# Kernel tuning notes

Hardware: AMD Instinct MI355X
Metric: run time of the kernel (lower is better)

## Reference

```python
import jax, jax.numpy as jnp
import numpy as np

TEMPERATURE = 0.07
EPS = 1e-08
HARD_NEG_WEIGHT = 2.0
DOMAIN_SEP_WEIGHT = 1.5


def setup_inputs() -> dict:
    key = jax.random.key(0)
    k1, k2, k3 = jax.random.split(key, 3)
    B, L, D = 32, 256, 256
    feats = jax.random.normal(k1, (B, L, D), dtype=jnp.float32)
    dataset_ids = jax.random.randint(k2, (B, L), 0, 4, dtype=jnp.int64 if jax.config.read('jax_enable_x64') else jnp.int32)
    image_ids = jax.random.randint(k3, (B, L), 0, 128, dtype=jnp.int64 if jax.config.read('jax_enable_x64') else jnp.int32)
    return {"feats": feats, "dataset_ids": dataset_ids, "image_ids": image_ids}


def reference(feats, dataset_ids, image_ids):
    B, L, D = feats.shape
    N = B * L
    x = feats.reshape(N, D)
    # F.normalize: x / clamp_min(||x||, eps)
    x = x / jnp.maximum(jnp.linalg.norm(x, axis=-1, keepdims=True), EPS)
    sim = jnp.matmul(x, x.T) / TEMPERATURE  # [N, N]

    did = dataset_ids.reshape(-1)
    iid = image_ids.reshape(-1)
    same_img = (did[:, None] == did[None, :]) & (iid[:, None] == iid[None, :])
    eye = jnp.eye(N, dtype=bool)
    pos_mask = same_img & ~eye
    diff_dataset = did[:, None] != did[None, :]

    sim_exp = jnp.exp(sim)

    # global 0.8-quantile over cross-dataset similarities (linear interpolation, as torch.quantile)
    q = jnp.nanquantile(jnp.where(diff_dataset, sim, jnp.nan), 0.8)
    thr = jnp.where(diff_dataset.any(), q, 0.0)
    hard_neg_mask = diff_dataset & (sim > thr)

    neg_weights = jnp.where(diff_dataset, DOMAIN_SEP_WEIGHT, 1.0) * jnp.where(hard_neg_mask, HARD_NEG_WEIGHT, 1.0)

    pos_sum = jnp.sum(sim_exp * pos_mask.astype(sim.dtype), axis=1)
    # note: ~pos_mask includes the diagonal, matching the torch code
    neg_sum = jnp.sum(sim_exp * neg_weights * (~pos_mask).astype(sim.dtype), axis=1)

    loss = -jnp.log((pos_sum + EPS) / (pos_sum + neg_sum + EPS))

    valid = pos_mask.any(axis=1)
    n_valid = valid.sum()
    masked_mean = jnp.sum(loss * valid.astype(loss.dtype)) / jnp.maximum(n_valid, 1).astype(loss.dtype)
    return jnp.where(n_valid > 0, masked_mean, loss.mean())
```

## Files before the change

kernel.cpp:

```cpp
#include <hip/hip_runtime.h>
#include <hip/hip_bf16.h>
#include <math.h>

#define N_TOK 8192
#define DIM   256
#define INV_T 14.285714285714286f
#define RANGE 14.2857142857f
#define EPS   1e-8f
#define NBINS 8192
#define LOG2E 1.44269504f

typedef __attribute__((ext_vector_type(4))) float f32x4;
typedef __attribute__((ext_vector_type(8))) short short8;

#define OFF_P     0
#define P_BYTES   (N_TOK * DIM * 2)
#define OFF_PP    (OFF_P + P_BYTES)
#define OFF_PN    (OFF_PP + 64 * N_TOK * 4)
#define OFF_HIST  (OFF_PN + 64 * N_TOK * 4)
#define OFF_THR   (OFF_HIST + NBINS * 4)
#define WS_USED   (OFF_THR + 256)

#define GLOBAL_AS __attribute__((address_space(1)))
#define LDS_AS    __attribute__((address_space(3)))

__device__ __forceinline__ void tri_decode(int b, int& it, int& jt) {
    int i_low = (int)((sqrtf(8.f * (float)b + 1.f) - 1.f) * 0.5f);
    while ((i_low + 1) * (i_low + 2) / 2 <= b) ++i_low;
    while (i_low * (i_low + 1) / 2 > b) --i_low;
    const int j_low = b - i_low * (i_low + 1) / 2;
    it = 63 - i_low; jt = 63 - j_low;
}

__global__ __launch_bounds__(256) void k_prep(const float* __restrict__ feats,
                                              __hip_bfloat16* __restrict__ P) {
    const int row = blockIdx.x * 4 + (threadIdx.x >> 6);
    const int l = threadIdx.x & 63;
    const float4 v = *reinterpret_cast<const float4*>(&feats[(size_t)row * DIM + l * 4]);
    float s = v.x * v.x + v.y * v.y + v.z * v.z + v.w * v.w;
#pragma unroll
    for (int m = 1; m <= 32; m <<= 1) s += __shfl_xor(s, m);
    const float r = 1.0f / fmaxf(sqrtf(s), EPS);
    ushort4 o;
    __hip_bfloat16 h;
    h = __float2bfloat16(v.x * r); o.x = *reinterpret_cast<unsigned short*>(&h);
    h = __float2bfloat16(v.y * r); o.y = *reinterpret_cast<unsigned short*>(&h);
    h = __float2bfloat16(v.z * r); o.z = *reinterpret_cast<unsigned short*>(&h);
    h = __float2bfloat16(v.w * r); o.w = *reinterpret_cast<unsigned short*>(&h);
    *reinterpret_cast<ushort4*>(&P[(size_t)row * DIM + l * 4]) = o;
}

__global__ __launch_bounds__(512, 4) void k_hist(
    const __hip_bfloat16* __restrict__ P, const int* __restrict__ did,
    unsigned int* __restrict__ hist) {
    int it, jt;
    tri_decode(blockIdx.x, it, jt);
    if (((it * 67 + jt * 31) & 31) != 0) return;
    const int iBase = it * 128, jBase = jt * 128;
    const bool diag = (it == jt);

    __shared__ __hip_bfloat16 At[128 * 64];
    __shared__ __hip_bfloat16 Bt[128 * 64];
    __shared__ int dA[128], dB[128];
    __shared__ unsigned int h[NBINS];

    const int tid = threadIdx.x;
    const int w = tid >> 6, l = tid & 63;
    const int wr = w >> 1, wc = w & 1;
    const int g = l >> 4, p = l & 15;

    if (tid < 128) dA[tid] = did[iBase + tid];
    else if (tid < 256) dB[tid - 128] = did[jBase + tid - 128];
    for (int i = tid; i < NBINS; i += 512) h[i] = 0;

    f32x4 acc[2][4];
#pragma unroll
    for (int a = 0; a < 2; a++)
#pragma unroll
        for (int c = 0; c < 4; c++) acc[a][c] = (f32x4){0.f, 0.f, 0.f, 0.f};

    const int rloc = l >> 3;
    const int swz = (((l & 7) ^ (rloc & 7)) << 4);
    const char* Pb = (const char*)P;

    for (int t = 0; t < 4; ++t) {
#pragma unroll
        for (int i_ = 0; i_ < 2; ++i_) {
            const int rowbase = w * 16 + i_ * 8;
            const char* srcA = Pb + (size_t)(iBase + rowbase + rloc) * 512 + t * 128 + swz;
            __builtin_amdgcn_global_load_lds(
                (const GLOBAL_AS unsigned int*)srcA,
                (LDS_AS unsigned int*)(&At[rowbase * 64]), 16, 0, 0);
            const char* srcB = Pb + (size_t)(jBase + rowbase + rloc) * 512 + t * 128 + swz;
            __builtin_amdgcn_global_load_lds(
                (const GLOBAL_AS unsigned int*)srcB,
                (LDS_AS unsigned int*)(&Bt[rowbase * 64]), 16, 0, 0);
        }
        __syncthreads();
#pragma unroll
        for (int ks = 0; ks < 2; ++ks) {
            short8 af[2], bf[4];
            const int cb = ks * 64 + (g << 4);
#pragma unroll
            for (int fm = 0; fm < 2; ++fm) {
                const int row = wr * 32 + fm * 16 + p;
                af[fm] = *reinterpret_cast<const short8*>(
                    (const char*)At + row * 128 + (cb ^ ((row & 7) << 4)));
            }
#pragma unroll
            for (int fn = 0; fn < 4; ++fn) {
                const int row = wc * 64 + fn * 16 + p;
                bf[fn] = *reinterpret_cast<const short8*>(
                    (const char*)Bt + row * 128 + (cb ^ ((row & 7) << 4)));
            }
#pragma unroll
            for (int fm = 0; fm < 2; ++fm)
#pragma unroll
                for (int fn = 0; fn < 4; ++fn)
                    acc[fm][fn] = __builtin_amdgcn_mfma_f32_16x16x32_bf16(
                        af[fm], bf[fn], acc[fm][fn], 0, 0, 0);
        }
        __syncthreads();
    }

    int dRow[2][4];
#pragma unroll
    for (int fm = 0; fm < 2; ++fm)
#pragma unroll
        for (int q = 0; q < 4; ++q) dRow[fm][q] = dA[wr * 32 + fm * 16 + g * 4 + q];

    const unsigned int wgt = diag ? 1u : 2u;
    const float binScale = (float)NBINS / (2.0f * RANGE);
    const float K1 = INV_T * binScale, K0 = RANGE * binScale;
#pragma unroll
    for (int fn = 0; fn < 4; ++fn) {
        const int dcol = dB[wc * 64 + fn * 16 + p];
#pragma unroll
        for (int fm = 0; fm < 2; ++fm)
#pragma unroll
            for (int q = 0; q < 4; ++q) {
                if (dRow[fm][q] != dcol) {
                    int bn = (int)fmaf(acc[fm][fn][q], K1, K0);
                    bn = min(max(bn, 0), NBINS - 1);
                    atomicAdd(&h[bn], wgt);
                }
            }
    }
    __syncthreads();
    for (int i = tid; i < NBINS; i += 512) {
        unsigned int c = h[i];
        if (c) atomicAdd(&hist[i], c);
    }
}

__global__ __launch_bounds__(512, 8) void k_main(
    const __hip_bfloat16* __restrict__ P,
    const int* __restrict__ did, const int* __restrict__ iid,
    const float* __restrict__ thrp,
    float* __restrict__ partP, float* __restrict__ partN) {
    int it, jt;
    tri_decode(blockIdx.x, it, jt);
    const int iBase = it * 128, jBase = jt * 128;
    const bool diag = (it == jt);

    __shared__ __hip_bfloat16 At[2][128 * 32];
    __shared__ __hip_bfloat16 Bt[2][128 * 32];
    __shared__ int dA[128], kA[128], dB[128], kB[128];
    __shared__ float rbT[2][128], rbP[2][128];
    __shared__ float cbT[4][128], cbP[4][128];

    const int tid = threadIdx.x;
    const int w = tid >> 6, l = tid & 63;
    const int wr = w >> 1, wc = w & 1;
    const int g = l >> 4, p = l & 15;

    if (tid < 128) {
        int d = did[iBase + tid], i2 = iid[iBase + tid];
        dA[tid] = d; kA[tid] = (d << 16) | i2;
    } else if (tid < 256) {
        int r = tid - 128;
        int d = did[jBase + r], i2 = iid[jBase + r];
        dB[r] = d; kB[r] = (d << 16) | i2;
    }

    f32x4 acc[2][4];
#pragma unroll
    for (int a = 0; a < 2; a++)
#pragma unroll
        for (int c = 0; c < 4; c++) acc[a][c] = (f32x4){0.f, 0.f, 0.f, 0.f};

    const int rloc = l >> 2;
    const int swzB = (((l & 3) ^ (rloc & 3)) << 4);
    const char* Pb = (const char*)P;

#define STAGE(buf, t)                                                             \
    {                                                                             \
        const int row_ = w * 16 + rloc;                                           \
        const char* srcA_ = Pb + (size_t)(iBase + row_) * 512 + (t) * 64 + swzB;  \
        __builtin_amdgcn_global_load_lds(                                         \
            (const GLOBAL_AS unsigned int*)srcA_,                                 \
            (LDS_AS unsigned int*)(&At[buf][(w * 16) * 32]), 16, 0, 0);           \
        const char* srcB_ = Pb + (size_t)(jBase + row_) * 512 + (t) * 64 + swzB;  \
        __builtin_amdgcn_global_load_lds(                                         \
            (const GLOBAL_AS unsigned int*)srcB_,                                 \
            (LDS_AS unsigned int*)(&Bt[buf][(w * 16) * 32]), 16, 0, 0);           \
    }

    STAGE(0, 0);
    __syncthreads();

    for (int t = 0; t < 8; ++t) {
        const int cur = t & 1;
        if (t < 7) STAGE(cur ^ 1, t + 1);
        short8 af[2], bf[4];
        const int cbg = g << 4;
#pragma unroll
        for (int fm = 0; fm < 2; ++fm) {
            const int row = wr * 32 + fm * 16 + p;
            af[fm] = *reinterpret_cast<const short8*>(
                (const char*)At[cur] + row * 64 + (cbg ^ ((row & 3) << 4)));
        }
#pragma unroll
        for (int fn = 0; fn < 4; ++fn) {
            const int row = wc * 64 + fn * 16 + p;
            bf[fn] = *reinterpret_cast<const short8*>(
                (const char*)Bt[cur] + row * 64 + (cbg ^ ((row & 3) << 4)));
        }
#pragma unroll
        for (int fm = 0; fm < 2; ++fm)
#pragma unroll
            for (int fn = 0; fn < 4; ++fn)
                acc[fm][fn] = __builtin_amdgcn_mfma_f32_16x16x32_bf16(
                    af[fm], bf[fn], acc[fm][fn], 0, 0, 0);
        __syncthreads();
    }
#undef STAGE

    int dRow[2][4], kRow[2][4], selfRow[2][4];
#pragma unroll
    for (int fm = 0; fm < 2; ++fm)
#pragma unroll
        for (int q = 0; q < 4; ++q) {
            const int rIdx = wr * 32 + fm * 16 + g * 4 + q;
            dRow[fm][q] = dA[rIdx];
            kRow[fm][q] = kA[rIdx];
            selfRow[fm][q] = diag ? rIdx : -1;
        }

    const float CE = INV_T * LOG2E;
    const float thr2 = thrp[0] * LOG2E;
    float tR[2][4], pR[2][4], tC[4], pC[4];
#pragma unroll
    for (int a = 0; a < 4; a++) { tC[a] = 0.f; pC[a] = 0.f; }
#pragma unroll
    for (int a = 0; a < 2; a++)
#pragma unroll
        for (int c = 0; c < 4; c++) { tR[a][c] = 0.f; pR[a][c] = 0.f; }

#pragma unroll
    for (int fn = 0; fn < 4; ++fn) {
        const int cIdx = wc * 64 + fn * 16 + p;
        const int dcol = dB[cIdx], kcol = kB[cIdx];
#pragma unroll
        for (int fm = 0; fm < 2; ++fm)
#pragma unroll
            for (int q = 0; q < 4; ++q) {
                const float tt = acc[fm][fn][q] * CE;
                const float e = __builtin_amdgcn_exp2f(tt);
                const float w1 = (tt > thr2) ? 3.0f : 1.5f;
                const float wg = (dRow[fm][q] != dcol) ? w1 : 1.0f;
                tR[fm][q] = fmaf(e, wg, tR[fm][q]);
                tC[fn] = fmaf(e, wg, tC[fn]);
                const bool pos = (kRow[fm][q] == kcol) && (selfRow[fm][q] != cIdx);
                const float ep = pos ? e : 0.f;
                pR[fm][q] += ep;
                pC[fn] += ep;
            }
    }
#pragma unroll
    for (int m = 1; m <= 8; m <<= 1)
#pragma unroll
        for (int a = 0; a < 2; a++)
#pragma unroll
            for (int c = 0; c < 4; c++) {
                tR[a][c] += __shfl_xor(tR[a][c], m);
                pR[a][c] += __shfl_xor(pR[a][c], m);
            }
#pragma unroll
    for (int m = 16; m <= 32; m <<= 1)
#pragma unroll
        for (int a = 0; a < 4; a++) {
            tC[a] += __shfl_xor(tC[a], m);
            pC[a] += __shfl_xor(pC[a], m);
        }
    float tv = 0.f, pv = 0.f;
#pragma unroll
    for (int fm = 0; fm < 2; ++fm)
#pragma unroll
        for (int q = 0; q < 4; ++q)
            if (p == fm * 4 + q) { tv = tR[fm][q]; pv = pR[fm][q]; }

    if (p < 8) {
        const int rowLocal = (p >> 2) * 16 + g * 4 + (p & 3);
        rbT[wc][wr * 32 + rowLocal] = tv;
        rbP[wc][wr * 32 + rowLocal] = pv;
    }
    if (l < 16) {
#pragma unroll
        for (int fn = 0; fn < 4; ++fn) {
            cbT[wr][wc * 64 + fn * 16 + l] = tC[fn];
            cbP[wr][wc * 64 + fn * 16 + l] = pC[fn];
        }
    }
    __syncthreads();
    if (tid < 128) {
        const float T = rbT[0][tid] + rbT[1][tid];
        const float Pp = rbP[0][tid] + rbP[1][tid];
        const size_t off = (size_t)jt * N_TOK + iBase + tid;
        partP[off] = Pp;
        partN[off] = T - Pp;
    } else if (tid < 256 && !diag) {
        const int c = tid - 128;
        const float T = cbT[0][c] + cbT[1][c] + cbT[2][c] + cbT[3][c];
        const float Pp = cbP[0][c] + cbP[1][c] + cbP[2][c] + cbP[3][c];
        const size_t off = (size_t)it * N_TOK + jBase + c;
        partP[off] = Pp;
        partN[off] = T - Pp;
    }
}

__global__ __launch_bounds__(1024) void k_thr(const unsigned int* __restrict__ hist,
                                              float* __restrict__ thrp) {
    __shared__ unsigned long long scan[1024];
    const int t = threadIdx.x;
    const int CHUNK = NBINS / 1024;
    const int base = t * CHUNK;
    unsigned long long own = 0;
    for (int i = 0; i < CHUNK; i++) own += hist[base + i];
    scan[t] = own;
    __syncthreads();
    for (int o = 1; o < 1024; o <<= 1) {
        unsigned long long v = (t >= o) ? scan[t - o] : 0ULL;
        __syncthreads();
        scan[t] += v;
        __syncthreads();
    }
    unsigned long long total = scan[1023];
    if (total == 0) {
        if (t == 0) thrp[0] = 0.f;
        return;
    }
    unsigned long long k1 = (4ULL * (total - 1)) / 5ULL;
    unsigned long long rem = (4ULL * (total - 1)) % 5ULL;
    float frac = (float)rem * 0.2f;
    unsigned long long k2 = (k1 + 1 < total) ? k1 + 1 : k1;
    __shared__ float vk[2];
    unsigned long long cumBefore = scan[t] - own;
    const float binw = 2.0f * RANGE / (float)NBINS;
    for (int which = 0; which < 2; which++) {
        unsigned long long k = which ? k2 : k1;
        if (cumBefore <= k && k < scan[t]) {
            unsigned long long c = cumBefore;
            int bin = base;
            for (int i = 0; i < CHUNK; i++) {
                c += hist[base + i];
                if (c > k) { bin = base + i; break; }
            }
            vk[which] = -RANGE + ((float)bin + 0.5f) * binw;
        }
    }
    __syncthreads();
    if (t == 0) thrp[0] = vk[0] + frac * (vk[1] - vk[0]);
}

__global__ __launch_bounds__(256) void k_reduce(const float* __restrict__ pp,
                                                const float* __restrict__ pn,
                                                float* __restrict__ acc) {
    const int t = threadIdx.x;
    const int r = blockIdx.x * 128 + (t & 127);
    const int jh = t >> 7;
    float sp = 0.f, sn = 0.f;
    const float* bp = pp + (size_t)jh * 32 * N_TOK + r;
    const float* bn = pn + (size_t)jh * 32 * N_TOK + r;
#pragma unroll 8
    for (int j = 0; j < 32; ++j) {
        sp += bp[(size_t)j * N_TOK];
        sn += bn[(size_t)j * N_TOK];
    }
    __shared__ float shp[128], shn[128];
    if (jh) { shp[t & 127] = sp; shn[t & 127] = sn; }
    __syncthreads();
    float sumV = 0.f, sumA = 0.f, cnt = 0.f;
    if (!jh) {
        const float p = sp + shp[t];
        const float n = sn + shn[t];
        const float loss = -logf((p + EPS) / (p + n + EPS));
        sumA = loss;
        if (p > 0.f) { sumV = loss; cnt = 1.f; }
    }
#pragma unroll
    for (int m = 1; m <= 32; m <<= 1) {
        sumV += __shfl_xor(sumV, m);
        sumA += __shfl_xor(sumA, m);
        cnt += __shfl_xor(cnt, m);
    }
    __shared__ float wv[4], wa[4], wn[4];
    if ((t & 63) == 0) { wv[t >> 6] = sumV; wa[t >> 6] = sumA; wn[t >> 6] = cnt; }
    __syncthreads();
    if (t == 0) {
        atomicAdd(&acc[0], wv[0] + wv[1] + wv[2] + wv[3]);
        atomicAdd(&acc[1], wa[0] + wa[1] + wa[2] + wa[3]);
        atomicAdd(&acc[2], wn[0] + wn[1] + wn[2] + wn[3]);
    }
}

__global__ __launch_bounds__(64) void k_last(const float* __restrict__ acc,
                                             float* __restrict__ out) {
    if (threadIdx.x == 0) {
        const float nv = acc[2];
        out[0] = (nv > 0.f) ? (acc[0] / fmaxf(nv, 1.f)) : (acc[1] / (float)N_TOK);
    }
}

extern "C" void kernel_launch(void* const* d_in, const int* in_sizes, int n_in,
                              void* d_out, int out_size, void* d_ws, size_t ws_size,
                              hipStream_t stream) {
    (void)in_sizes; (void)n_in; (void)out_size; (void)ws_size;
    const float* feats = (const float*)d_in[0];
    const int* did = (const int*)d_in[1];
    const int* iid = (const int*)d_in[2];
    char* ws = (char*)d_ws;
    __hip_bfloat16* P = (__hip_bfloat16*)(ws + OFF_P);
    float* partP = (float*)(ws + OFF_PP);
    float* partN = (float*)(ws + OFF_PN);
    unsigned int* hist = (unsigned int*)(ws + OFF_HIST);
    float* thrp = (float*)(ws + OFF_THR);
    float* accum = (float*)(ws + OFF_THR + 16);

    hipMemsetAsync(ws + OFF_HIST, 0, NBINS * 4 + 256, stream);
    k_prep<<<N_TOK / 4, 256, 0, stream>>>(feats, P);
    const int NTILES = 64 * 65 / 2;
    k_hist<<<NTILES, 512, 0, stream>>>(P, did, hist);
    k_thr<<<1, 1024, 0, stream>>>(hist, thrp);
    k_main<<<NTILES, 512, 0, stream>>>(P, did, iid, thrp, partP, partN);
    k_reduce<<<64, 256, 0, stream>>>(partP, partN, accum);
    k_last<<<1, 64, 0, stream>>>(accum, (float*)d_out);
}
```

Measured before the change: 79.26 us.

## Switch normalized features to FP8 and use single-stage FP8 MFMA GEMM

Quantizes the normalized features to FP8 instead of bf16 and runs the similarity GEMMs with FP8 MFMA instructions. The whole 128x256 tile for each operand is staged into padded LDS in one pass, replacing the double-buffered k-loop. The histogram kernel now launches only the sampled tiles (65 blocks) instead of launching every tile and exiting early. The diagonal exp is replaced with an exact constant to hide FP8 self-similarity error. FP8 precision can change the similarity values and the quantile threshold, which risks accuracy, and the larger LDS footprint lowers occupancy.

New measurement: 72.92 us. 8.0% less time.

```diff
diff --git a/kernel.cpp b/kernel.cpp
--- a/kernel.cpp
+++ b/kernel.cpp
@@ -1,5 +1,4 @@
 #include <hip/hip_runtime.h>
-#include <hip/hip_bf16.h>
 #include <math.h>
 
 #define N_TOK 8192
@@ -11,18 +10,20 @@
 #define LOG2E 1.44269504f
 
 typedef __attribute__((ext_vector_type(4))) float f32x4;
-typedef __attribute__((ext_vector_type(8))) short short8;
 
 #define OFF_P     0
-#define P_BYTES   (N_TOK * DIM * 2)
+#define P_BYTES   (N_TOK * DIM)
 #define OFF_PP    (OFF_P + P_BYTES)
 #define OFF_PN    (OFF_PP + 64 * N_TOK * 4)
 #define OFF_HIST  (OFF_PN + 64 * N_TOK * 4)
 #define OFF_THR   (OFF_HIST + NBINS * 4)
-#define WS_USED   (OFF_THR + 256)
 
 #define GLOBAL_AS __attribute__((address_space(1)))
 #define LDS_AS    __attribute__((address_space(3)))
+
+#define ROWB 272
+#define SLOTS_PER_MAT (128 * 17)
+#define STAGE_CALLS (2 * SLOTS_PER_MAT / 64)
 
 __device__ __forceinline__ void tri_decode(int b, int& it, int& jt) {
     int i_low = (int)((sqrtf(8.f * (float)b + 1.f) - 1.f) * 0.5f);
@@ -33,7 +34,7 @@
 }
 
 __global__ __launch_bounds__(256) void k_prep(const float* __restrict__ feats,
-                                              __hip_bfloat16* __restrict__ P) {
+                                              unsigned int* __restrict__ Pq) {
     const int row = blockIdx.x * 4 + (threadIdx.x >> 6);
     const int l = threadIdx.x & 63;
     const float4 v = *reinterpret_cast<const float4*>(&feats[(size_t)row * DIM + l * 4]);
@@ -41,88 +42,83 @@
 #pragma unroll
     for (int m = 1; m <= 32; m <<= 1) s += __shfl_xor(s, m);
     const float r = 1.0f / fmaxf(sqrtf(s), EPS);
-    ushort4 o;
-    __hip_bfloat16 h;
-    h = __float2bfloat16(v.x * r); o.x = *reinterpret_cast<unsigned short*>(&h);
-    h = __float2bfloat16(v.y * r); o.y = *reinterpret_cast<unsigned short*>(&h);
-    h = __float2bfloat16(v.z * r); o.z = *reinterpret_cast<unsigned short*>(&h);
-    h = __float2bfloat16(v.w * r); o.w = *reinterpret_cast<unsigned short*>(&h);
-    *reinterpret_cast<ushort4*>(&P[(size_t)row * DIM + l * 4]) = o;
-}
-
-__global__ __launch_bounds__(512, 4) void k_hist(
-    const __hip_bfloat16* __restrict__ P, const int* __restrict__ did,
+    int pk = __builtin_amdgcn_cvt_pk_fp8_f32(v.x * r, v.y * r, 0, false);
+    pk = __builtin_amdgcn_cvt_pk_fp8_f32(v.z * r, v.w * r, pk, true);
+    Pq[row * 64 + l] = (unsigned int)pk;
+}
+
+__device__ __forceinline__ void stage_and_gemm(
+    const char* __restrict__ Pq, int iBase, int jBase,
+    char* At, char* Bt, int tid, f32x4 (&acc)[2][4]) {
+    const int w = tid >> 6, l = tid & 63;
+    for (int k = w; k < STAGE_CALLS; k += 8) {
+        const int s0 = k * 64;
+        const int isB = (s0 >= SLOTS_PER_MAT);
+        const int r0 = s0 - (isB ? SLOTS_PER_MAT : 0);
+        const int sl = r0 + l;
+        const int row = sl / 17;
+        const int col = sl - row * 17;
+        const int gb = isB ? jBase : iBase;
+        const char* src = Pq + (size_t)(gb + row) * DIM + (col & 15) * 16;
+        char* dst = (isB ? Bt : At) + (size_t)r0 * 16;
+        __builtin_amdgcn_global_load_lds((const GLOBAL_AS unsigned int*)src,
+                                         (LDS_AS unsigned int*)dst, 16, 0, 0);
+    }
+    __syncthreads();
+
+    const int wr = w >> 1, wc = w & 1;
+    const int g = l >> 4, p = l & 15;
+    const char* a0 = At + (wr * 32 + p) * ROWB + g * 8;
+    const char* b0 = Bt + (wc * 64 + p) * ROWB + g * 8;
+#pragma unroll
+    for (int c = 0; c < 8; ++c) {
+        const int off = c * 32;
+        const long af0 = *(const long*)(a0 + off);
+        const long af1 = *(const long*)(a0 + 16 * ROWB + off);
+        const long bf0 = *(const long*)(b0 + off);
+        const long bf1 = *(const long*)(b0 + 16 * ROWB + off);
+        const long bf2 = *(const long*)(b0 + 32 * ROWB + off);
+        const long bf3 = *(const long*)(b0 + 48 * ROWB + off);
+        acc[0][0] = __builtin_amdgcn_mfma_f32_16x16x32_fp8_fp8(af0, bf0, acc[0][0], 0, 0, 0);
+        acc[0][1] = __builtin_amdgcn_mfma_f32_16x16x32_fp8_fp8(af0, bf1, acc[0][1], 0, 0, 0);
+        acc[0][2] = __builtin_amdgcn_mfma_f32_16x16x32_fp8_fp8(af0, bf2, acc[0][2], 0, 0, 0);
+        acc[0][3] = __builtin_amdgcn_mfma_f32_16x16x32_fp8_fp8(af0, bf3, acc[0][3], 0, 0, 0);
+        acc[1][0] = __builtin_amdgcn_mfma_f32_16x16x32_fp8_fp8(af1, bf0, acc[1][0], 0, 0, 0);
+        acc[1][1] = __builtin_amdgcn_mfma_f32_16x16x32_fp8_fp8(af1, bf1, acc[1][1], 0, 0, 0);
+        acc[1][2] = __builtin_amdgcn_mfma_f32_16x16x32_fp8_fp8(af1, bf2, acc[1][2], 0, 0, 0);
+        acc[1][3] = __builtin_amdgcn_mfma_f32_16x16x32_fp8_fp8(af1, bf3, acc[1][3], 0, 0, 0);
+    }
+}
+
+__global__ __launch_bounds__(512, 2) void k_hist(
+    const char* __restrict__ Pq, const int* __restrict__ did,
     unsigned int* __restrict__ hist) {
     int it, jt;
-    tri_decode(blockIdx.x, it, jt);
-    if (((it * 67 + jt * 31) & 31) != 0) return;
+    tri_decode(blockIdx.x * 32, it, jt);
     const int iBase = it * 128, jBase = jt * 128;
     const bool diag = (it == jt);
 
-    __shared__ __hip_bfloat16 At[128 * 64];
-    __shared__ __hip_bfloat16 Bt[128 * 64];
+    __shared__ char At[SLOTS_PER_MAT * 16];
+    __shared__ char Bt[SLOTS_PER_MAT * 16];
     __shared__ int dA[128], dB[128];
     __shared__ unsigned int h[NBINS];
 
     const int tid = threadIdx.x;
+    if (tid < 128) dA[tid] = did[iBase + tid];
+    else if (tid < 256) dB[tid - 128] = did[jBase + tid - 128];
+    for (int i = tid; i < NBINS; i += 512) h[i] = 0;
+
+    f32x4 acc[2][4];
+#pragma unroll
+    for (int a = 0; a < 2; a++)
+#pragma unroll
+        for (int c = 0; c < 4; c++) acc[a][c] = (f32x4){0.f, 0.f, 0.f, 0.f};
+
+    stage_and_gemm(Pq, iBase, jBase, At, Bt, tid, acc);
+
     const int w = tid >> 6, l = tid & 63;
     const int wr = w >> 1, wc = w & 1;
     const int g = l >> 4, p = l & 15;
-
-    if (tid < 128) dA[tid] = did[iBase + tid];
-    else if (tid < 256) dB[tid - 128] = did[jBase + tid - 128];
-    for (int i = tid; i < NBINS; i += 512) h[i] = 0;
-
-    f32x4 acc[2][4];
-#pragma unroll
-    for (int a = 0; a < 2; a++)
-#pragma unroll
-        for (int c = 0; c < 4; c++) acc[a][c] = (f32x4){0.f, 0.f, 0.f, 0.f};
-
-    const int rloc = l >> 3;
-    const int swz = (((l & 7) ^ (rloc & 7)) << 4);
-    const char* Pb = (const char*)P;
-
-    for (int t = 0; t < 4; ++t) {
-#pragma unroll
-        for (int i_ = 0; i_ < 2; ++i_) {
-            const int rowbase = w * 16 + i_ * 8;
-            const char* srcA = Pb + (size_t)(iBase + rowbase + rloc) * 512 + t * 128 + swz;
-            __builtin_amdgcn_global_load_lds(
-                (const GLOBAL_AS unsigned int*)srcA,
-                (LDS_AS unsigned int*)(&At[rowbase * 64]), 16, 0, 0);
-            const char* srcB = Pb + (size_t)(jBase + rowbase + rloc) * 512 + t * 128 + swz;
-            __builtin_amdgcn_global_load_lds(
-                (const GLOBAL_AS unsigned int*)srcB,
-                (LDS_AS unsigned int*)(&Bt[rowbase * 64]), 16, 0, 0);
-        }
-        __syncthreads();
-#pragma unroll
-        for (int ks = 0; ks < 2; ++ks) {
-            short8 af[2], bf[4];
-            const int cb = ks * 64 + (g << 4);
-#pragma unroll
-            for (int fm = 0; fm < 2; ++fm) {
-                const int row = wr * 32 + fm * 16 + p;
-                af[fm] = *reinterpret_cast<const short8*>(
-                    (const char*)At + row * 128 + (cb ^ ((row & 7) << 4)));
-            }
-#pragma unroll
-            for (int fn = 0; fn < 4; ++fn) {
-                const int row = wc * 64 + fn * 16 + p;
-                bf[fn] = *reinterpret_cast<const short8*>(
-                    (const char*)Bt + row * 128 + (cb ^ ((row & 7) << 4)));
-            }
-#pragma unroll
-            for (int fm = 0; fm < 2; ++fm)
-#pragma unroll
-                for (int fn = 0; fn < 4; ++fn)
-                    acc[fm][fn] = __builtin_amdgcn_mfma_f32_16x16x32_bf16(
-                        af[fm], bf[fn], acc[fm][fn], 0, 0, 0);
-        }
-        __syncthreads();
-    }
-
     int dRow[2][4];
 #pragma unroll
     for (int fm = 0; fm < 2; ++fm)
@@ -153,8 +149,8 @@
     }
 }
 
-__global__ __launch_bounds__(512, 8) void k_main(
-    const __hip_bfloat16* __restrict__ P,
+__global__ __launch_bounds__(512, 4) void k_main(
+    const char* __restrict__ Pq,
     const int* __restrict__ did, const int* __restrict__ iid,
     const float* __restrict__ thrp,
     float* __restrict__ partP, float* __restrict__ partN) {
@@ -163,17 +159,13 @@
     const int iBase = it * 128, jBase = jt * 128;
     const bool diag = (it == jt);
 
-    __shared__ __hip_bfloat16 At[2][128 * 32];
-    __shared__ __hip_bfloat16 Bt[2][128 * 32];
+    __shared__ char At[SLOTS_PER_MAT * 16];
+    __shared__ char Bt[SLOTS_PER_MAT * 16];
     __shared__ int dA[128], kA[128], dB[128], kB[128];
     __shared__ float rbT[2][128], rbP[2][128];
     __shared__ float cbT[4][128], cbP[4][128];
 
     const int tid = threadIdx.x;
-    const int w = tid >> 6, l = tid & 63;
-    const int wr = w >> 1, wc = w & 1;
-    const int g = l >> 4, p = l & 15;
-
     if (tid < 128) {
         int d = did[iBase + tid], i2 = iid[iBase + tid];
         dA[tid] = d; kA[tid] = (d << 16) | i2;
@@ -189,52 +181,11 @@
 #pragma unroll
         for (int c = 0; c < 4; c++) acc[a][c] = (f32x4){0.f, 0.f, 0.f, 0.f};
 
-    const int rloc = l >> 2;
-    const int swzB = (((l & 3) ^ (rloc & 3)) << 4);
-    const char* Pb = (const char*)P;
-
-#define STAGE(buf, t)                                                             \
-    {                                                                             \
-        const int row_ = w * 16 + rloc;                                           \
-        const char* srcA_ = Pb + (size_t)(iBase + row_) * 512 + (t) * 64 + swzB;  \
-        __builtin_amdgcn_global_load_lds(                                         \
-            (const GLOBAL_AS unsigned int*)srcA_,                                 \
-            (LDS_AS unsigned int*)(&At[buf][(w * 16) * 32]), 16, 0, 0);           \
-        const char* srcB_ = Pb + (size_t)(jBase + row_) * 512 + (t) * 64 + swzB;  \
-        __builtin_amdgcn_global_load_lds(                                         \
-            (const GLOBAL_AS unsigned int*)srcB_,                                 \
-            (LDS_AS unsigned int*)(&Bt[buf][(w * 16) * 32]), 16, 0, 0);           \
-    }
-
-    STAGE(0, 0);
-    __syncthreads();
-
-    for (int t = 0; t < 8; ++t) {
-        const int cur = t & 1;
-        if (t < 7) STAGE(cur ^ 1, t + 1);
-        short8 af[2], bf[4];
-        const int cbg = g << 4;
-#pragma unroll
-        for (int fm = 0; fm < 2; ++fm) {
-            const int row = wr * 32 + fm * 16 + p;
-            af[fm] = *reinterpret_cast<const short8*>(
-                (const char*)At[cur] + row * 64 + (cbg ^ ((row & 3) << 4)));
-        }
-#pragma unroll
-        for (int fn = 0; fn < 4; ++fn) {
-            const int row = wc * 64 + fn * 16 + p;
-            bf[fn] = *reinterpret_cast<const short8*>(
-                (const char*)Bt[cur] + row * 64 + (cbg ^ ((row & 3) << 4)));
-        }
-#pragma unroll
-        for (int fm = 0; fm < 2; ++fm)
-#pragma unroll
-            for (int fn = 0; fn < 4; ++fn)
-                acc[fm][fn] = __builtin_amdgcn_mfma_f32_16x16x32_bf16(
-                    af[fm], bf[fn], acc[fm][fn], 0, 0, 0);
-        __syncthreads();
-    }
-#undef STAGE
+    stage_and_gemm(Pq, iBase, jBase, At, Bt, tid, acc);
+
+    const int w = tid >> 6, l = tid & 63;
+    const int wr = w >> 1, wc = w & 1;
+    const int g = l >> 4, p = l & 15;
 
     int dRow[2][4], kRow[2][4], selfRow[2][4];
 #pragma unroll
@@ -249,6 +200,7 @@
 
     const float CE = INV_T * LOG2E;
     const float thr2 = thrp[0] * LOG2E;
+    const float E_DIAG = __builtin_amdgcn_exp2f(CE);
     float tR[2][4], pR[2][4], tC[4], pC[4];
 #pragma unroll
     for (int a = 0; a < 4; a++) { tC[a] = 0.f; pC[a] = 0.f; }
@@ -266,12 +218,14 @@
 #pragma unroll
             for (int q = 0; q < 4; ++q) {
                 const float tt = acc[fm][fn][q] * CE;
-                const float e = __builtin_amdgcn_exp2f(tt);
+                float e = __builtin_amdgcn_exp2f(tt);
+                const bool self = (selfRow[fm][q] == cIdx);
+                e = self ? E_DIAG : e;
                 const float w1 = (tt > thr2) ? 3.0f : 1.5f;
                 const float wg = (dRow[fm][q] != dcol) ? w1 : 1.0f;
                 tR[fm][q] = fmaf(e, wg, tR[fm][q]);
                 tC[fn] = fmaf(e, wg, tC[fn]);
-                const bool pos = (kRow[fm][q] == kcol) && (selfRow[fm][q] != cIdx);
+                const bool pos = (kRow[fm][q] == kcol) && !self;
                 const float ep = pos ? e : 0.f;
                 pR[fm][q] += ep;
                 pC[fn] += ep;
@@ -430,7 +384,7 @@
     const int* did = (const int*)d_in[1];
     const int* iid = (const int*)d_in[2];
     char* ws = (char*)d_ws;
-    __hip_bfloat16* P = (__hip_bfloat16*)(ws + OFF_P);
+    char* Pq = ws + OFF_P;
     float* partP = (float*)(ws + OFF_PP);
     float* partN = (float*)(ws + OFF_PN);
     unsigned int* hist = (unsigned int*)(ws + OFF_HIST);
@@ -438,11 +392,10 @@
     float* accum = (float*)(ws + OFF_THR + 16);
 
     hipMemsetAsync(ws + OFF_HIST, 0, NBINS * 4 + 256, stream);
-    k_prep<<<N_TOK / 4, 256, 0, stream>>>(feats, P);
-    const int NTILES = 64 * 65 / 2;
-    k_hist<<<NTILES, 512, 0, stream>>>(P, did, hist);
+    k_prep<<<N_TOK / 4, 256, 0, stream>>>(feats, (unsigned int*)Pq);
+    k_hist<<<65, 512, 0, stream>>>(Pq, did, hist);
     k_thr<<<1, 1024, 0, stream>>>(hist, thrp);
-    k_main<<<NTILES, 512, 0, stream>>>(P, did, iid, thrp, partP, partN);
+    k_main<<<64 * 65 / 2, 512, 0, stream>>>(Pq, did, iid, thrp, partP, partN);
     k_reduce<<<64, 256, 0, stream>>>(partP, partN, accum);
     k_last<<<1, 64, 0, stream>>>(accum, (float*)d_out);
 }
```
